# Kernel optimization log

Hardware: AMD Instinct MI355X
Metric: run time of the kernel (lower is better)

The kernel has to match this reference:

```python
import jax, jax.numpy as jnp
import numpy as np

TWO_PI = 2.0 * np.pi
N_T = 12     # 3 * n_blocks
K = 16       # n_mixture
H = 256      # hidden width
MIN_W = 0.01
RAMP_P = 2
EPS = 1e-6


def setup_inputs() -> dict:
    key = jax.random.key(0)
    ks = jax.random.split(key, 4)
    B, L = 64, 3072
    z = jax.random.uniform(ks[0], (B, L, 1), dtype=jnp.float32) * TWO_PI

    def w(k, shape, fan_in, scale=1.0):
        return jax.random.normal(k, shape, dtype=jnp.float32) * (scale / np.sqrt(fan_in))

    W1 = w(ks[1], (N_T, 2, H), 2)
    b1 = jnp.zeros((N_T, H), jnp.float32)
    W2 = w(ks[2], (N_T, H, H), H)
    b2 = jnp.zeros((N_T, H), jnp.float32)
    W3 = w(ks[3], (N_T, H, 3 * K), H, scale=0.1)
    b3 = jnp.zeros((N_T, 3 * K), jnp.float32)
    return {"z": z, "W1": W1, "b1": b1, "W2": W2, "b2": b2, "W3": W3, "b3": b3}


def _mod_2pi(x):
    return jnp.remainder(x, TWO_PI)


def _flow(z, W1, b1, W2, b2, W3, b3):
    B, L, _ = z.shape
    n = L // 3
    base = jnp.arange(n) * 3
    ldj_total = jnp.zeros((B,), z.dtype)
    for t in range(N_T):
        off = (0, 2, 1)[t % 3]          # mask.roll(-1) each iteration
        idx = base + off                 # active-site indices (replaces boolean mask)
        zr = jnp.roll(z, 1, axis=1)
        V = _mod_2pi(z - zr)             # (B, L, 1) link variables
        c1 = V[:, (idx - 1) % L]         # V.roll(+1,1)[:, mask]  (B, n, 1)
        c2 = V[:, (idx + 2) % L]         # V.roll(-2,1)[:, mask]  (B, n, 1)
        ctx = jnp.concatenate([c1, c2], axis=-1)   # (B, n, 2)
        # pointwise conditioner MLP (Tanh)
        h = jnp.tanh(ctx @ W1[t] + b1[t])
        h = jnp.tanh(h @ W2[t] + b2[t])
        params = h @ W3[t] + b3[t]                 # (B, n, 3K)
        log_scale, shift, wlogit = jnp.split(params, 3, axis=-1)
        alpha = jnp.exp(log_scale)                 # (B, n, K)
        wgt = jax.nn.softmax(wlogit, axis=-1) * (1.0 - K * MIN_W) + MIN_W
        # weighted mixture-of-sigmoids transform on u = x / 2pi with ramp(u) = u^p/(u^p+(1-u)^p)
        u = jnp.clip(V[:, idx, 0] / TWO_PI, EPS, 1.0 - EPS)   # (B, n)
        a = u ** RAMP_P
        b_ = (1.0 - u) ** RAMP_P
        s = a / (a + b_)
        ds_du = RAMP_P * u ** (RAMP_P - 1) * (1.0 - u) ** (RAMP_P - 1) / (a + b_) ** 2
        s = jnp.clip(s, EPS, 1.0 - EPS)
        logit_s = jnp.log(s) - jnp.log1p(-s)
        g = jax.nn.sigmoid(alpha * (logit_s[..., None] + shift))   # (B, n, K)
        y = jnp.sum(wgt * g, axis=-1)                              # (B, n) in (0,1)
        dy_ds = jnp.sum(wgt * alpha * g * (1.0 - g), axis=-1) / (s * (1.0 - s))
        dy_du = dy_ds * ds_du                                      # = dy_angle/dx_angle
        ldj_total = ldj_total + jnp.sum(jnp.log(dy_du), axis=1)
        # phi = where(mask, mod_2pi(U + z.roll(+1)), z): only active sites change
        phi_vals = _mod_2pi(TWO_PI * y[..., None] + zr[:, idx])
        z = z.at[:, idx].set(phi_vals)
    return z, ldj_total


def reference(z, W1, b1, W2, b2, W3, b3):
    return _flow(z, W1, b1, W2, b2, W3, b3)
```

## Files before the change

### kernel.cpp

```cpp
#include <hip/hip_runtime.h>
#include <math.h>

#define L_DIM 3072
#define B_DIM 64
#define H_DIM 256
#define HP2 260
#define PP 49
#define TWO_PI_F 6.28318530717958647692f
#define EPS_F 1e-6f

__device__ __forceinline__ float mod2pi(float x){
    float q = floorf(x * (1.0f/TWO_PI_F));
    return fmaf(-TWO_PI_F, q, x);
}

__device__ __forceinline__ float fast_tanh(float x){
    float t = __expf(2.0f*x);
    return 1.0f - __fdividef(2.0f, t + 1.0f);
}

__global__ __launch_bounds__(256) void init_kernel(const float* __restrict__ zin, float* __restrict__ out){
    int i = blockIdx.x*256 + threadIdx.x;
    if (i < B_DIM*L_DIM) out[i] = zin[i];
    if (i < B_DIM) out[B_DIM*L_DIM + i] = 0.0f;
}

__global__ __launch_bounds__(256) void round_kernel(
    float* __restrict__ z, float* __restrict__ ldj,
    const float* __restrict__ W1, const float* __restrict__ b1,
    const float* __restrict__ W2, const float* __restrict__ b2,
    const float* __restrict__ W3, const float* __restrict__ b3,
    int off)
{
    __shared__ float h_lds[64*HP2];
    __shared__ float p_lds[64*PP];
    __shared__ float c1_l[64], c2_l[64], u_l[64], zr_l[64];

    const int tid = threadIdx.x;
    const int bid = blockIdx.x;
    const int b  = bid >> 4;
    const int j0 = (bid & 15) << 6;
    float* zb = z + b*L_DIM;

    if (tid < 64){
        int idx = 3*(j0 + tid) + off;
        int im2 = idx-2; if (im2 < 0) im2 += L_DIM;
        int im1 = idx-1; if (im1 < 0) im1 += L_DIM;
        int ip1 = idx+1; if (ip1 >= L_DIM) ip1 -= L_DIM;
        int ip2 = idx+2; if (ip2 >= L_DIM) ip2 -= L_DIM;
        float zi  = zb[idx];
        float zm1 = zb[im1];
        float zm2 = zb[im2];
        float zp1 = zb[ip1];
        float zp2 = zb[ip2];
        c1_l[tid] = mod2pi(zm1 - zm2);
        c2_l[tid] = mod2pi(zp2 - zp1);
        float V   = mod2pi(zi - zm1);
        float u = V * (1.0f/TWO_PI_F);
        u_l[tid] = fminf(fmaxf(u, EPS_F), 1.0f-EPS_F);
        zr_l[tid] = zm1;
    }
    __syncthreads();

    {
        float w0 = W1[tid];
        float w1 = W1[H_DIM + tid];
        float bb = b1[tid];
        #pragma unroll 8
        for (int m=0; m<64; m++){
            float pre = fmaf(c1_l[m], w0, fmaf(c2_l[m], w1, bb));
            h_lds[m*HP2 + tid] = fast_tanh(pre);
        }
    }
    __syncthreads();

    const int wv   = tid >> 6;
    const int lane = tid & 63;
    const int ty = lane >> 4;
    const int tx = lane & 15;
    const int c4 = wv*16 + tx;

    float acc[16][4];
    #pragma unroll
    for (int s=0; s<16; s++){ acc[s][0]=0.f; acc[s][1]=0.f; acc[s][2]=0.f; acc[s][3]=0.f; }

    const float4* __restrict__ W2v = (const float4*)W2;
    for (int k=0; k<H_DIM; k+=4){
        float4 wq0 = W2v[(k+0)*64 + c4];
        float4 wq1 = W2v[(k+1)*64 + c4];
        float4 wq2 = W2v[(k+2)*64 + c4];
        float4 wq3 = W2v[(k+3)*64 + c4];
        #pragma unroll
        for (int half=0; half<2; half++){
            float4 av[8];
            #pragma unroll
            for (int s=0; s<8; s++)
                av[s] = *(const float4*)&h_lds[((half*8+s)*4+ty)*HP2 + k];
            #pragma unroll
            for (int s=0; s<8; s++){
                const int ss = half*8 + s;
                acc[ss][0] = fmaf(av[s].x, wq0.x, acc[ss][0]);
                acc[ss][1] = fmaf(av[s].x, wq0.y, acc[ss][1]);
                acc[ss][2] = fmaf(av[s].x, wq0.z, acc[ss][2]);
                acc[ss][3] = fmaf(av[s].x, wq0.w, acc[ss][3]);
                acc[ss][0] = fmaf(av[s].y, wq1.x, acc[ss][0]);
                acc[ss][1] = fmaf(av[s].y, wq1.y, acc[ss][1]);
                acc[ss][2] = fmaf(av[s].y, wq1.z, acc[ss][2]);
                acc[ss][3] = fmaf(av[s].y, wq1.w, acc[ss][3]);
                acc[ss][0] = fmaf(av[s].z, wq2.x, acc[ss][0]);
                acc[ss][1] = fmaf(av[s].z, wq2.y, acc[ss][1]);
                acc[ss][2] = fmaf(av[s].z, wq2.z, acc[ss][2]);
                acc[ss][3] = fmaf(av[s].z, wq2.w, acc[ss][3]);
                acc[ss][0] = fmaf(av[s].w, wq3.x, acc[ss][0]);
                acc[ss][1] = fmaf(av[s].w, wq3.y, acc[ss][1]);
                acc[ss][2] = fmaf(av[s].w, wq3.z, acc[ss][2]);
                acc[ss][3] = fmaf(av[s].w, wq3.w, acc[ss][3]);
            }
        }
    }
    __syncthreads();

    {
        const int n0 = wv*64 + tx*4;
        float4 bb = *(const float4*)&b2[n0];
        #pragma unroll
        for (int s=0; s<16; s++){
            int m = s*4 + ty;
            float4 o;
            o.x = fast_tanh(acc[s][0] + bb.x);
            o.y = fast_tanh(acc[s][1] + bb.y);
            o.z = fast_tanh(acc[s][2] + bb.z);
            o.w = fast_tanh(acc[s][3] + bb.w);
            *(float4*)&h_lds[m*HP2 + n0] = o;
        }
    }
    __syncthreads();

    {
        const int m4 = tid & 63;
        const int ol = __builtin_amdgcn_readfirstlane(tid >> 6);
        float acc3[12];
        #pragma unroll
        for (int r=0; r<12; r++) acc3[r] = 0.f;
        const float4* __restrict__ W3v = (const float4*)W3;
        for (int k=0; k<H_DIM; k+=4){
            float4 hv = *(const float4*)&h_lds[m4*HP2 + k];
            float hw[4] = {hv.x, hv.y, hv.z, hv.w};
            #pragma unroll
            for (int j=0; j<4; j++){
                float h = hw[j];
                float4 q0 = W3v[(k+j)*12 + ol*3 + 0];
                float4 q1 = W3v[(k+j)*12 + ol*3 + 1];
                float4 q2 = W3v[(k+j)*12 + ol*3 + 2];
                acc3[0] = fmaf(h, q0.x, acc3[0]);  acc3[1] = fmaf(h, q0.y, acc3[1]);
                acc3[2] = fmaf(h, q0.z, acc3[2]);  acc3[3] = fmaf(h, q0.w, acc3[3]);
                acc3[4] = fmaf(h, q1.x, acc3[4]);  acc3[5] = fmaf(h, q1.y, acc3[5]);
                acc3[6] = fmaf(h, q1.z, acc3[6]);  acc3[7] = fmaf(h, q1.w, acc3[7]);
                acc3[8] = fmaf(h, q2.x, acc3[8]);  acc3[9] = fmaf(h, q2.y, acc3[9]);
                acc3[10]= fmaf(h, q2.z, acc3[10]); acc3[11]= fmaf(h, q2.w, acc3[11]);
            }
        }
        #pragma unroll
        for (int r=0; r<12; r++)
            p_lds[m4*PP + ol*12 + r] = acc3[r] + b3[ol*12 + r];
    }
    __syncthreads();

    float ll = 0.0f;
    if (tid < 64){
        const float* p = p_lds + tid*PP;
        float mx = p[32];
        #pragma unroll
        for (int i=1; i<16; i++) mx = fmaxf(mx, p[32+i]);
        float w[16]; float se = 0.0f;
        #pragma unroll
        for (int i=0; i<16; i++){ w[i] = __expf(p[32+i]-mx); se += w[i]; }
        float inv = __fdividef(0.84f, se);

        float u = u_l[tid];
        float a  = u*u;
        float om = 1.0f - u;
        float b_ = om*om;
        float apb = a + b_;
        float s = __fdividef(a, apb);
        float ds_du = __fdividef(2.0f*u*om, apb*apb);
        s = fminf(fmaxf(s, EPS_F), 1.0f-EPS_F);
        float logit_s = __logf(s) - log1pf(-s);

        float y = 0.0f, dd = 0.0f;
        #pragma unroll
        for (int i=0; i<16; i++){
            float alpha = __expf(p[i]);
            float wgt = fmaf(w[i], inv, 0.01f);
            float targ = alpha * (logit_s + p[16+i]);
            float g = __fdividef(1.0f, 1.0f + __expf(-targ));
            y  = fmaf(wgt, g, y);
            dd = fmaf(wgt*alpha, g*(1.0f-g), dd);
        }
        float dy_du = __fdividef(dd, s*(1.0f-s)) * ds_du;
        ll = __logf(dy_du);

        int idx = 3*(j0 + tid) + off;
        zb[idx] = mod2pi(fmaf(TWO_PI_F, y, zr_l[tid]));
    }
    if (tid < 64){
        #pragma unroll
        for (int o=32; o>0; o>>=1) ll += __shfl_down(ll, o, 64);
        if (tid == 0) atomicAdd(&ldj[b], ll);
    }
}

extern "C" void kernel_launch(void* const* d_in, const int* in_sizes, int n_in,
                              void* d_out, int out_size, void* d_ws, size_t ws_size,
                              hipStream_t stream) {
    const float* z_in = (const float*)d_in[0];
    const float* W1 = (const float*)d_in[1];
    const float* b1 = (const float*)d_in[2];
    const float* W2 = (const float*)d_in[3];
    const float* b2 = (const float*)d_in[4];
    const float* W3 = (const float*)d_in[5];
    const float* b3 = (const float*)d_in[6];
    float* out = (float*)d_out;
    float* zbuf = out;
    float* ldj  = out + B_DIM*L_DIM;

    init_kernel<<<(B_DIM*L_DIM + 255)/256, 256, 0, stream>>>(z_in, out);

    for (int t=0; t<12; t++){
        int r = t % 3;
        int off = (r==0) ? 0 : ((r==1) ? 2 : 1);
        round_kernel<<<1024, 256, 0, stream>>>(
            zbuf, ldj,
            W1 + t*2*H_DIM, b1 + t*H_DIM,
            W2 + t*H_DIM*H_DIM, b2 + t*H_DIM,
            W3 + t*H_DIM*48, b3 + t*48,
            off);
    }
}
```

Before: 1.940 ms.

## Retile layer-2 GEMM to 8x8 register tiles with prefetched W2 loads

Changes the per-thread register tile of the 64x256x256 hidden-layer matmul from 16 rows x 4 columns to 8 rows x 8 columns. This lowers the number of LDS reads per FMA, since each float4 activation read now feeds 8 outputs instead of 4. It also software-pipelines the global W2 loads one k-step ahead and adds a min-blocks-per-CU hint to launch_bounds. The cost is more live registers for the double-buffered weights, and the 8-column stride may cause LDS bank conflicts when the tanh outputs are written back.

```diff
diff --git a/kernel.cpp b/kernel.cpp
--- a/kernel.cpp
+++ b/kernel.cpp
@@ -25,7 +25,7 @@
     if (i < B_DIM) out[B_DIM*L_DIM + i] = 0.0f;
 }
 
-__global__ __launch_bounds__(256) void round_kernel(
+__global__ __launch_bounds__(256, 2) void round_kernel(
     float* __restrict__ z, float* __restrict__ ldj,
     const float* __restrict__ W1, const float* __restrict__ b1,
     const float* __restrict__ W2, const float* __restrict__ b2,
@@ -76,69 +76,85 @@
 
     const int wv   = tid >> 6;
     const int lane = tid & 63;
-    const int ty = lane >> 4;
-    const int tx = lane & 15;
-    const int c4 = wv*16 + tx;
-
-    float acc[16][4];
+    const int ty = lane >> 3;
+    const int tx = lane & 7;
+    const int c4 = wv*16 + tx*2;
+
+    float acc[8][8];
     #pragma unroll
-    for (int s=0; s<16; s++){ acc[s][0]=0.f; acc[s][1]=0.f; acc[s][2]=0.f; acc[s][3]=0.f; }
+    for (int s=0; s<8; s++)
+        #pragma unroll
+        for (int c=0; c<8; c++) acc[s][c] = 0.f;
 
     const float4* __restrict__ W2v = (const float4*)W2;
+    float4 wq[4][2];
+    #pragma unroll
+    for (int j=0; j<4; j++){
+        wq[j][0] = W2v[j*64 + c4];
+        wq[j][1] = W2v[j*64 + c4 + 1];
+    }
+
     for (int k=0; k<H_DIM; k+=4){
-        float4 wq0 = W2v[(k+0)*64 + c4];
-        float4 wq1 = W2v[(k+1)*64 + c4];
-        float4 wq2 = W2v[(k+2)*64 + c4];
-        float4 wq3 = W2v[(k+3)*64 + c4];
-        #pragma unroll
-        for (int half=0; half<2; half++){
-            float4 av[8];
+        float4 av[8];
+        #pragma unroll
+        for (int s=0; s<8; s++)
+            av[s] = *(const float4*)&h_lds[(s*8+ty)*HP2 + k];
+        int kn = k + 4; if (kn >= H_DIM) kn = 0;
+        float4 wqn[4][2];
+        #pragma unroll
+        for (int j=0; j<4; j++){
+            wqn[j][0] = W2v[(kn+j)*64 + c4];
+            wqn[j][1] = W2v[(kn+j)*64 + c4 + 1];
+        }
+        #pragma unroll
+        for (int s=0; s<8; s++){
+            float a4[4] = {av[s].x, av[s].y, av[s].z, av[s].w};
             #pragma unroll
-            for (int s=0; s<8; s++)
-                av[s] = *(const float4*)&h_lds[((half*8+s)*4+ty)*HP2 + k];
-            #pragma unroll
-            for (int s=0; s<8; s++){
-                const int ss = half*8 + s;
-                acc[ss][0] = fmaf(av[s].x, wq0.x, acc[ss][0]);
-                acc[ss][1] = fmaf(av[s].x, wq0.y, acc[ss][1]);
-                acc[ss][2] = fmaf(av[s].x, wq0.z, acc[ss][2]);
-                acc[ss][3] = fmaf(av[s].x, wq0.w, acc[ss][3]);
-                acc[ss][0] = fmaf(av[s].y, wq1.x, acc[ss][0]);
-                acc[ss][1] = fmaf(av[s].y, wq1.y, acc[ss][1]);
-                acc[ss][2] = fmaf(av[s].y, wq1.z, acc[ss][2]);
-                acc[ss][3] = fmaf(av[s].y, wq1.w, acc[ss][3]);
-                acc[ss][0] = fmaf(av[s].z, wq2.x, acc[ss][0]);
-                acc[ss][1] = fmaf(av[s].z, wq2.y, acc[ss][1]);
-                acc[ss][2] = fmaf(av[s].z, wq2.z, acc[ss][2]);
-                acc[ss][3] = fmaf(av[s].z, wq2.w, acc[ss][3]);
-                acc[ss][0] = fmaf(av[s].w, wq3.x, acc[ss][0]);
-                acc[ss][1] = fmaf(av[s].w, wq3.y, acc[ss][1]);
-                acc[ss][2] = fmaf(av[s].w, wq3.z, acc[ss][2]);
-                acc[ss][3] = fmaf(av[s].w, wq3.w, acc[ss][3]);
+            for (int j=0; j<4; j++){
+                float a = a4[j];
+                acc[s][0] = fmaf(a, wq[j][0].x, acc[s][0]);
+                acc[s][1] = fmaf(a, wq[j][0].y, acc[s][1]);
+                acc[s][2] = fmaf(a, wq[j][0].z, acc[s][2]);
+                acc[s][3] = fmaf(a, wq[j][0].w, acc[s][3]);
+                acc[s][4] = fmaf(a, wq[j][1].x, acc[s][4]);
+                acc[s][5] = fmaf(a, wq[j][1].y, acc[s][5]);
+                acc[s][6] = fmaf(a, wq[j][1].z, acc[s][6]);
+                acc[s][7] = fmaf(a, wq[j][1].w, acc[s][7]);
             }
         }
+        #pragma unroll
+        for (int j=0; j<4; j++){
+            wq[j][0] = wqn[j][0];
+            wq[j][1] = wqn[j][1];
+        }
     }
     __syncthreads();
 
     {
-        const int n0 = wv*64 + tx*4;
-        float4 bb = *(const float4*)&b2[n0];
-        #pragma unroll
-        for (int s=0; s<16; s++){
-            int m = s*4 + ty;
-            float4 o;
-            o.x = fast_tanh(acc[s][0] + bb.x);
-            o.y = fast_tanh(acc[s][1] + bb.y);
-            o.z = fast_tanh(acc[s][2] + bb.z);
-            o.w = fast_tanh(acc[s][3] + bb.w);
-            *(float4*)&h_lds[m*HP2 + n0] = o;
+        const int n0 = wv*64 + tx*8;
+        float4 bb0 = *(const float4*)&b2[n0];
+        float4 bb1 = *(const float4*)&b2[n0+4];
+        #pragma unroll
+        for (int s=0; s<8; s++){
+            int m = s*8 + ty;
+            float4 o0, o1;
+            o0.x = fast_tanh(acc[s][0] + bb0.x);
+            o0.y = fast_tanh(acc[s][1] + bb0.y);
+            o0.z = fast_tanh(acc[s][2] + bb0.z);
+            o0.w = fast_tanh(acc[s][3] + bb0.w);
+            o1.x = fast_tanh(acc[s][4] + bb1.x);
+            o1.y = fast_tanh(acc[s][5] + bb1.y);
+            o1.z = fast_tanh(acc[s][6] + bb1.z);
+            o1.w = fast_tanh(acc[s][7] + bb1.w);
+            *(float4*)&h_lds[m*HP2 + n0]     = o0;
+            *(float4*)&h_lds[m*HP2 + n0 + 4] = o1;
         }
     }
     __syncthreads();
 
     {
-        const int m4 = tid & 63;
-        const int ol = __builtin_amdgcn_readfirstlane(tid >> 6);
+        const int m4 = lane;
+        const int ol = __builtin_amdgcn_readfirstlane(wv);
         float acc3[12];
         #pragma unroll
         for (int r=0; r<12; r++) acc3[r] = 0.f;
```

After: 5.065 ms. +161.2%, slower.

## Remap layer-2 GEMM so each lane owns a row with wave-uniform weight loads

Applied to the files above, without the earlier changes.

The hidden-layer matmul is rewritten so each lane computes one sample row across 64 output columns, with the wave index made wave-uniform via readfirstlane. W2 loads become uniform across the wave (scalar/broadcast loads) and each lane streams its own h row from LDS with a one-step prefetch. The previous 4x16 thread tile with per-lane vector weight loads is dropped. Launch bounds now request 2 blocks per SM, which constrains registers while holding 64 accumulators per thread and may cause spills.

```diff
diff --git a/kernel.cpp b/kernel.cpp
--- a/kernel.cpp
+++ b/kernel.cpp
@@ -25,7 +25,7 @@
     if (i < B_DIM) out[B_DIM*L_DIM + i] = 0.0f;
 }
 
-__global__ __launch_bounds__(256) void round_kernel(
+__global__ __launch_bounds__(256, 2) void round_kernel(
     float* __restrict__ z, float* __restrict__ ldj,
     const float* __restrict__ W1, const float* __restrict__ b1,
     const float* __restrict__ W2, const float* __restrict__ b2,
@@ -36,7 +36,9 @@
     __shared__ float p_lds[64*PP];
     __shared__ float c1_l[64], c2_l[64], u_l[64], zr_l[64];
 
-    const int tid = threadIdx.x;
+    const int tid  = threadIdx.x;
+    const int lane = tid & 63;
+    const int wv_u = __builtin_amdgcn_readfirstlane(tid >> 6);
     const int bid = blockIdx.x;
     const int b  = bid >> 4;
     const int j0 = (bid & 15) << 6;
@@ -74,84 +76,62 @@
     }
     __syncthreads();
 
-    const int wv   = tid >> 6;
-    const int lane = tid & 63;
-    const int ty = lane >> 4;
-    const int tx = lane & 15;
-    const int c4 = wv*16 + tx;
-
-    float acc[16][4];
+    float acc[64];
     #pragma unroll
-    for (int s=0; s<16; s++){ acc[s][0]=0.f; acc[s][1]=0.f; acc[s][2]=0.f; acc[s][3]=0.f; }
-
-    const float4* __restrict__ W2v = (const float4*)W2;
-    for (int k=0; k<H_DIM; k+=4){
-        float4 wq0 = W2v[(k+0)*64 + c4];
-        float4 wq1 = W2v[(k+1)*64 + c4];
-        float4 wq2 = W2v[(k+2)*64 + c4];
-        float4 wq3 = W2v[(k+3)*64 + c4];
-        #pragma unroll
-        for (int half=0; half<2; half++){
-            float4 av[8];
+    for (int c=0; c<64; c++) acc[c] = 0.f;
+
+    {
+        const float* __restrict__ W2w = W2 + wv_u*64;
+        float4 h4 = *(const float4*)&h_lds[lane*HP2];
+        for (int k=0; k<H_DIM; k+=4){
+            float4 h4n = *(const float4*)&h_lds[lane*HP2 + ((k+4) & (H_DIM-1))];
+            float hk[4] = {h4.x, h4.y, h4.z, h4.w};
             #pragma unroll
-            for (int s=0; s<8; s++)
-                av[s] = *(const float4*)&h_lds[((half*8+s)*4+ty)*HP2 + k];
-            #pragma unroll
-            for (int s=0; s<8; s++){
-                const int ss = half*8 + s;
-                acc[ss][0] = fmaf(av[s].x, wq0.x, acc[ss][0]);
-                acc[ss][1] = fmaf(av[s].x, wq0.y, acc[ss][1]);
-                acc[ss][2] = fmaf(av[s].x, wq0.z, acc[ss][2]);
-                acc[ss][3] = fmaf(av[s].x, wq0.w, acc[ss][3]);
-                acc[ss][0] = fmaf(av[s].y, wq1.x, acc[ss][0]);
-                acc[ss][1] = fmaf(av[s].y, wq1.y, acc[ss][1]);
-                acc[ss][2] = fmaf(av[s].y, wq1.z, acc[ss][2]);
-                acc[ss][3] = fmaf(av[s].y, wq1.w, acc[ss][3]);
-                acc[ss][0] = fmaf(av[s].z, wq2.x, acc[ss][0]);
-                acc[ss][1] = fmaf(av[s].z, wq2.y, acc[ss][1]);
-                acc[ss][2] = fmaf(av[s].z, wq2.z, acc[ss][2]);
-                acc[ss][3] = fmaf(av[s].z, wq2.w, acc[ss][3]);
-                acc[ss][0] = fmaf(av[s].w, wq3.x, acc[ss][0]);
-                acc[ss][1] = fmaf(av[s].w, wq3.y, acc[ss][1]);
-                acc[ss][2] = fmaf(av[s].w, wq3.z, acc[ss][2]);
-                acc[ss][3] = fmaf(av[s].w, wq3.w, acc[ss][3]);
+            for (int j=0; j<4; j++){
+                const float* wrow = W2w + (k+j)*H_DIM;
+                #pragma unroll
+                for (int q=0; q<16; q++){
+                    float4 wq = *(const float4*)(wrow + q*4);
+                    acc[q*4+0] = fmaf(hk[j], wq.x, acc[q*4+0]);
+                    acc[q*4+1] = fmaf(hk[j], wq.y, acc[q*4+1]);
+                    acc[q*4+2] = fmaf(hk[j], wq.z, acc[q*4+2]);
+                    acc[q*4+3] = fmaf(hk[j], wq.w, acc[q*4+3]);
+                }
             }
-        }
-    }
-    __syncthreads();
-
-    {
-        const int n0 = wv*64 + tx*4;
-        float4 bb = *(const float4*)&b2[n0];
-        #pragma unroll
-        for (int s=0; s<16; s++){
-            int m = s*4 + ty;
+            h4 = h4n;
+        }
+    }
+    __syncthreads();
+
+    {
+        const int n0 = wv_u*64;
+        #pragma unroll
+        for (int q=0; q<16; q++){
+            float4 bb = *(const float4*)&b2[n0 + q*4];
             float4 o;
-            o.x = fast_tanh(acc[s][0] + bb.x);
-            o.y = fast_tanh(acc[s][1] + bb.y);
-            o.z = fast_tanh(acc[s][2] + bb.z);
-            o.w = fast_tanh(acc[s][3] + bb.w);
-            *(float4*)&h_lds[m*HP2 + n0] = o;
-        }
-    }
-    __syncthreads();
-
-    {
-        const int m4 = tid & 63;
-        const int ol = __builtin_amdgcn_readfirstlane(tid >> 6);
+            o.x = fast_tanh(acc[q*4+0] + bb.x);
+            o.y = fast_tanh(acc[q*4+1] + bb.y);
+            o.z = fast_tanh(acc[q*4+2] + bb.z);
+            o.w = fast_tanh(acc[q*4+3] + bb.w);
+            *(float4*)&h_lds[lane*HP2 + n0 + q*4] = o;
+        }
+    }
+    __syncthreads();
+
+    {
         float acc3[12];
         #pragma unroll
         for (int r=0; r<12; r++) acc3[r] = 0.f;
         const float4* __restrict__ W3v = (const float4*)W3;
         for (int k=0; k<H_DIM; k+=4){
-            float4 hv = *(const float4*)&h_lds[m4*HP2 + k];
+            float4 hv = *(const float4*)&h_lds[lane*HP2 + k];
             float hw[4] = {hv.x, hv.y, hv.z, hv.w};
             #pragma unroll
             for (int j=0; j<4; j++){
                 float h = hw[j];
-                float4 q0 = W3v[(k+j)*12 + ol*3 + 0];
-                float4 q1 = W3v[(k+j)*12 + ol*3 + 1];
-                float4 q2 = W3v[(k+j)*12 + ol*3 + 2];
+                float4 q0 = W3v[(k+j)*12 + wv_u*3 + 0];
+                float4 q1 = W3v[(k+j)*12 + wv_u*3 + 1];
+                float4 q2 = W3v[(k+j)*12 + wv_u*3 + 2];
                 acc3[0] = fmaf(h, q0.x, acc3[0]);  acc3[1] = fmaf(h, q0.y, acc3[1]);
                 acc3[2] = fmaf(h, q0.z, acc3[2]);  acc3[3] = fmaf(h, q0.w, acc3[3]);
                 acc3[4] = fmaf(h, q1.x, acc3[4]);  acc3[5] = fmaf(h, q1.y, acc3[5]);
@@ -162,7 +142,7 @@
         }
         #pragma unroll
         for (int r=0; r<12; r++)
-            p_lds[m4*PP + ol*12 + r] = acc3[r] + b3[ol*12 + r];
+            p_lds[lane*PP + wv_u*12 + r] = acc3[r] + b3[wv_u*12 + r];
     }
     __syncthreads();
 
```

New measurement: 2.593 ms. 1.34x slower.
